# Kernel optimization log

Hardware: AMD Instinct MI355X
Metric: run time of the kernel (lower is better)

## Reference

```python
import jax, jax.numpy as jnp
import numpy as np

N = 50000
NEG_SLOPE = 0.2  # PyG GATConv default negative_slope


def _gat_layer(x, src, dst, edge_attr, W, We, a_src, a_dst, a_edge, bias):
    """Single-head PyG GATConv (heads=1, concat=True, add_self_loops=True,
    fill_value='mean' for self-loop edge_attr, dropout inactive / eval mode)."""
    n = x.shape[0]
    # add self loops; self-loop edge_attr = per-feature mean of edge_attr
    loop = jnp.arange(n)
    src2 = jnp.concatenate([src, loop])
    dst2 = jnp.concatenate([dst, loop])
    ea_loop = jnp.broadcast_to(edge_attr.mean(axis=0, keepdims=True), (n, edge_attr.shape[1]))
    ea = jnp.concatenate([edge_attr, ea_loop], axis=0)          # [E', edge_dim]

    h = x @ W                                                    # [N, C_out]
    a_s = h @ a_src                                              # [N]
    a_d = h @ a_dst                                              # [N]
    a_e = (ea @ We) @ a_edge                                     # [E']

    alpha = jax.nn.leaky_relu(a_s[src2] + a_d[dst2] + a_e, NEG_SLOPE)  # [E']
    # segment softmax over incoming edges of each dst node
    amax = jax.ops.segment_max(alpha, dst2, num_segments=n)     # [N]
    ex = jnp.exp(alpha - amax[dst2])                             # [E']
    denom = jax.ops.segment_sum(ex, dst2, num_segments=n)       # [N]
    w = ex / denom[dst2]                                         # [E']

    msg = h[src2] * w[:, None]                                   # [E', C_out]
    out = jax.ops.segment_sum(msg, dst2, num_segments=n) + bias  # [N, C_out]
    return out


def setup_inputs() -> dict:
    key = jax.random.key(0)
    ks = jax.random.split(key, 16)
    E, C_in, C_h, C_out, Ed = 800000, 128, 256, 128, 8
    s = 0.05
    inp = {
        "x": jax.random.normal(ks[0], (N, C_in), dtype=jnp.float32),
        "edge_index": jax.random.randint(ks[1], (2, E), 0, N, dtype=jnp.int32),
        "edge_attr": jax.random.normal(ks[2], (E, Ed), dtype=jnp.float32),
        # layer 1 params
        "W1": jax.random.normal(ks[3], (C_in, C_h), dtype=jnp.float32) * s,
        "We1": jax.random.normal(ks[4], (Ed, C_h), dtype=jnp.float32) * s,
        "as1": jax.random.normal(ks[5], (C_h,), dtype=jnp.float32) * s,
        "ad1": jax.random.normal(ks[6], (C_h,), dtype=jnp.float32) * s,
        "ae1": jax.random.normal(ks[7], (C_h,), dtype=jnp.float32) * s,
        "b1": jnp.zeros((C_h,), dtype=jnp.float32),
        # layer 2 params
        "W2": jax.random.normal(ks[8], (C_h, C_out), dtype=jnp.float32) * s,
        "We2": jax.random.normal(ks[9], (Ed, C_out), dtype=jnp.float32) * s,
        "as2": jax.random.normal(ks[10], (C_out,), dtype=jnp.float32) * s,
        "ad2": jax.random.normal(ks[11], (C_out,), dtype=jnp.float32) * s,
        "ae2": jax.random.normal(ks[12], (C_out,), dtype=jnp.float32) * s,
        "b2": jnp.zeros((C_out,), dtype=jnp.float32),
    }
    return inp


def reference(x, edge_index, edge_attr, W1, We1, as1, ad1, ae1, b1,
              W2, We2, as2, ad2, ae2, b2):
    src, dst = edge_index[0], edge_index[1]
    h = _gat_layer(x, src, dst, edge_attr, W1, We1, as1, ad1, ae1, b1)
    h = jax.nn.relu(h)  # relu between layers, not after last
    out = _gat_layer(h, src, dst, edge_attr, W2, We2, as2, ad2, ae2, b2)
    return out
```

## Files before the change

kernel.cpp:

```cpp
#include <hip/hip_runtime.h>
#include <hip/hip_bf16.h>


#define NEG_SLOPE 0.2f

typedef unsigned short u16;
typedef short short8 __attribute__((ext_vector_type(8)));
typedef float v4f __attribute__((ext_vector_type(4)));
typedef u16 u16x4 __attribute__((ext_vector_type(4)));
typedef u16 u16x8 __attribute__((ext_vector_type(8)));

__device__ __forceinline__ u16 f2bf(float f) {
    unsigned u = __float_as_uint(f);
    return (u16)((u + 0x7fffu + ((u >> 16) & 1u)) >> 16);
}
__device__ __forceinline__ float bf2f(u16 h) {
    return __uint_as_float(((unsigned)h) << 16);
}
__device__ __forceinline__ float bf_lo(int v) { return __uint_as_float(((unsigned)v) << 16); }
__device__ __forceinline__ float bf_hi(int v) { return __uint_as_float(((unsigned)v) & 0xffff0000u); }
__device__ __forceinline__ float lrelu(float x) {
    return x >= 0.f ? x : NEG_SLOPE * x;
}
__device__ __forceinline__ int ld_acq(int* p) {
    return __hip_atomic_load(p, __ATOMIC_ACQUIRE, __HIP_MEMORY_SCOPE_AGENT);
}
__device__ __forceinline__ void st_rel(int* p, int v) {
    __hip_atomic_store(p, v, __ATOMIC_RELEASE, __HIP_MEMORY_SCOPE_AGENT);
}

__global__ __launch_bounds__(256) void prep_kernel(
        const float* __restrict__ W1, u16* __restrict__ w1thi, u16* __restrict__ w1tlo,
        const float* __restrict__ W2, u16* __restrict__ w2thi, u16* __restrict__ w2tlo,
        const float* __restrict__ We1, const float* __restrict__ ae1v,
        const float* __restrict__ We2, const float* __restrict__ ae2v,
        float* __restrict__ we_vec1g, float* __restrict__ we_vec2g) {
    int tid = threadIdx.x;
    if (blockIdx.x < 256) {
        int t = blockIdx.x * 256 + tid;
        if (t < 128 * 256) {
            int k = t >> 8, m = t & 255;
            float v = W1[t];
            u16 h = f2bf(v);
            w1thi[(size_t)m * 128 + k] = h;
            w1tlo[(size_t)m * 128 + k] = f2bf(v - bf2f(h));
        } else {
            t -= 128 * 256;
            int k = t >> 7, m = t & 127;
            float v = W2[t];
            u16 h = f2bf(v);
            w2thi[(size_t)m * 256 + k] = h;
            w2tlo[(size_t)m * 256 + k] = f2bf(v - bf2f(h));
        }
        return;
    }
    __shared__ float wv[16];
    if (tid < 16) wv[tid] = 0.f;
    __syncthreads();
    {
        float a1 = ae1v[tid];
        int lane = tid & 63;
#pragma unroll
        for (int j = 0; j < 8; ++j) {
            float v = We1[j * 256 + tid] * a1;
#pragma unroll
            for (int o = 32; o; o >>= 1) v += __shfl_down(v, o);
            if (lane == 0) atomicAdd(&wv[j], v);
        }
        if (tid < 128) {
            float a2 = ae2v[tid];
#pragma unroll
            for (int j = 0; j < 8; ++j) {
                float v = We2[j * 128 + tid] * a2;
#pragma unroll
                for (int o = 32; o; o >>= 1) v += __shfl_down(v, o);
                if (lane == 0) atomicAdd(&wv[8 + j], v);
            }
        }
    }
    __syncthreads();
    if (tid < 8)  we_vec1g[tid] = wv[tid];
    else if (tid < 16) we_vec2g[tid - 8] = wv[tid];
}

#define BK 32
#define LDA 40
__global__ __launch_bounds__(256) void fat1_kernel(
        const float* __restrict__ ea, const int* __restrict__ dst,
        float* __restrict__ mean_acc, int* __restrict__ deg,
        int* __restrict__ rank, float2* __restrict__ aEe, int E,
        const float* __restrict__ we_vec1g, const float* __restrict__ we_vec2g,
        int Fb,
        const float* __restrict__ A32,
        const u16* __restrict__ Bh_g, const u16* __restrict__ Bl_g,
        u16* __restrict__ Cb, int Nrows, int K, int M,
        const float* __restrict__ av, const float* __restrict__ bv,
        float* __restrict__ as_out, float* __restrict__ ad_out, int gx) {
    __shared__ u16 Ah[64 * LDA], Bh[64 * LDA], Bl[64 * LDA];
    int tid = threadIdx.x;
    if ((int)blockIdx.x < Fb) {
        __shared__ float red[8];
        __shared__ float wv[16];
        if (tid < 16) { wv[tid] = (tid < 8) ? we_vec1g[tid] : we_vec2g[tid - 8];
                        if (tid < 8) red[tid] = 0.f; }
        __syncthreads();
        int e = (int)blockIdx.x * 256 + tid;
        float s[8] = {0.f};
        if (e < E) {
            const float4 v0 = *(const float4*)&ea[(size_t)e * 8];
            const float4 v1 = *(const float4*)&ea[(size_t)e * 8 + 4];
            int d = dst[e];
            s[0] = v0.x; s[1] = v0.y; s[2] = v0.z; s[3] = v0.w;
            s[4] = v1.x; s[5] = v1.y; s[6] = v1.z; s[7] = v1.w;
            float s1 = v0.x * wv[0] + v0.y * wv[1] + v0.z * wv[2] + v0.w * wv[3]
                     + v1.x * wv[4] + v1.y * wv[5] + v1.z * wv[6] + v1.w * wv[7];
            float s2 = v0.x * wv[8] + v0.y * wv[9] + v0.z * wv[10] + v0.w * wv[11]
                     + v1.x * wv[12] + v1.y * wv[13] + v1.z * wv[14] + v1.w * wv[15];
            aEe[e] = make_float2(s1, s2);
            rank[e] = atomicAdd(&deg[d << 4], 1);
        }
        int lane = tid & 63;
#pragma unroll
        for (int j = 0; j < 8; ++j) {
#pragma unroll
            for (int o = 32; o; o >>= 1) s[j] += __shfl_down(s[j], o);
            if (lane == 0) atomicAdd(&red[j], s[j]);
        }
        __syncthreads();
        if (tid < 8) atomicAdd(&mean_acc[tid], red[tid]);
        return;
    }
    int gb = (int)blockIdx.x - Fb;
    int lane = tid & 63;
    int wvx = tid >> 6;
    int l15 = lane & 15, quad = lane >> 4;
    int rb = (gb / gx) * 64;
    int cb = (gb % gx) * 64;

    v4f acc[4];
#pragma unroll
    for (int ni = 0; ni < 4; ++ni) acc[ni] = (v4f){0.f, 0.f, 0.f, 0.f};

    int sr = tid >> 2;
    int sc = (tid & 3) * 8;

    for (int kc = 0; kc < K; kc += BK) {
        int gr = rb + sr;
        u16x8 a0 = {0,0,0,0,0,0,0,0};
        if (gr < Nrows) {
            const float* pa = A32 + (size_t)gr * K + kc + sc;
            float4 f0 = *(const float4*)pa;
            float4 f1 = *(const float4*)(pa + 4);
            a0 = (u16x8){f2bf(f0.x), f2bf(f0.y), f2bf(f0.z), f2bf(f0.w),
                         f2bf(f1.x), f2bf(f1.y), f2bf(f1.z), f2bf(f1.w)};
        }
        size_t bb = (size_t)(cb + sr) * K + kc + sc;
        u16x8 b0 = *(const u16x8*)(Bh_g + bb);
        u16x8 b1 = *(const u16x8*)(Bl_g + bb);
        *(u16x8*)&Ah[sr * LDA + sc] = a0;
        *(u16x8*)&Bh[sr * LDA + sc] = b0;
        *(u16x8*)&Bl[sr * LDA + sc] = b1;
        __syncthreads();
        short8 ah = *(const short8*)&Ah[(wvx * 16 + l15) * LDA + quad * 8];
        short8 bh[4], bl[4];
#pragma unroll
        for (int ni = 0; ni < 4; ++ni) {
            int r = (ni * 16 + l15) * LDA + quad * 8;
            bh[ni] = *(const short8*)&Bh[r];
            bl[ni] = *(const short8*)&Bl[r];
        }
#pragma unroll
        for (int ni = 0; ni < 4; ++ni) {
            acc[ni] = __builtin_amdgcn_mfma_f32_16x16x32_bf16(ah, bh[ni], acc[ni], 0, 0, 0);
            acc[ni] = __builtin_amdgcn_mfma_f32_16x16x32_bf16(ah, bl[ni], acc[ni], 0, 0, 0);
        }
        __syncthreads();
    }
#pragma unroll
    for (int ni = 0; ni < 4; ++ni)
#pragma unroll
        for (int reg = 0; reg < 4; ++reg) {
            int row = rb + wvx * 16 + quad * 4 + reg;
            if (row < Nrows)
                Cb[(size_t)row * M + cb + ni * 16 + l15] = f2bf(acc[ni][reg]);
        }
    float sd[4] = {}, dd[4] = {};
#pragma unroll
    for (int ni = 0; ni < 4; ++ni) {
        int col = cb + ni * 16 + l15;
        float a = av[col], b = bv[col];
#pragma unroll
        for (int reg = 0; reg < 4; ++reg) {
            sd[reg] += acc[ni][reg] * a;
            dd[reg] += acc[ni][reg] * b;
        }
    }
#pragma unroll
    for (int off = 1; off < 16; off <<= 1)
#pragma unroll
        for (int reg = 0; reg < 4; ++reg) {
            sd[reg] += __shfl_xor(sd[reg], off);
            dd[reg] += __shfl_xor(dd[reg], off);
        }
    if (l15 == 0) {
        int row0 = rb + wvx * 16 + quad * 4;
#pragma unroll
        for (int reg = 0; reg < 4; ++reg)
            if (row0 + reg < Nrows) {
                atomicAdd(as_out + row0 + reg, sd[reg]);
                atomicAdd(ad_out + row0 + reg, dd[reg]);
            }
    }
}

__global__ __launch_bounds__(256) void scan_fused_kernel(
        const int* __restrict__ deg, int* __restrict__ row_start,
        int* __restrict__ partials, int* __restrict__ pprefix,
        int* __restrict__ gcount, int* __restrict__ gflag, int N, int n,
        const float* __restrict__ mean_acc, float Einv,
        const float* __restrict__ we_vec1, const float* __restrict__ we_vec2,
        float* __restrict__ ae_loop) {
    __shared__ int s[256];
    __shared__ int amLast, bprefix;
    int t = threadIdx.x, bid = blockIdx.x;
    int i = bid * 256 + t;
    int v = (i < N) ? deg[i << 4] : 0;
    s[t] = v; __syncthreads();
    for (int off = 1; off < 256; off <<= 1) {
        int u = (t >= off) ? s[t - off] : 0;
        __syncthreads();
        s[t] += u;
        __syncthreads();
    }
    int incl = s[t];
    int total = s[255];
    if (t == 0) {
        partials[bid] = total;
        __threadfence();
        int c = __hip_atomic_fetch_add(gcount, 1, __ATOMIC_ACQ_REL, __HIP_MEMORY_SCOPE_AGENT);
        amLast = (c == (int)gridDim.x - 1);
    }
    __syncthreads();
    if (amLast) {
        int G = gridDim.x;
        int pv = (t < G) ? ld_acq(&partials[t]) : 0;
        __syncthreads();
        s[t] = pv; __syncthreads();
        for (int off = 1; off < 256; off <<= 1) {
            int u = (t >= off) ? s[t - off] : 0;
            __syncthreads();
            s[t] += u;
            __syncthreads();
        }
        if (t < G) pprefix[t] = s[t] - pv;
        if (t == 0) {
            float s1 = 0.f, s2 = 0.f;
#pragma unroll
            for (int j = 0; j < 8; ++j) {
                float m = mean_acc[j] * Einv;
                s1 += m * we_vec1[j];
                s2 += m * we_vec2[j];
            }
            ae_loop[0] = s1; ae_loop[1] = s2;
        }
        __threadfence();
        __syncthreads();
        if (t == 0) st_rel(gflag, 1);
    }
    if (t == 0) {
        while (ld_acq(gflag) == 0) __builtin_amdgcn_s_sleep(2);
        bprefix = ld_acq(&pprefix[bid]);
    }
    __syncthreads();
    int ex = bprefix + incl - v;
    if (i < n) row_start[i] = ex;
}

__global__ __launch_bounds__(256) void fill_kernel(
        const int* __restrict__ src, const int* __restrict__ dst,
        const float2* __restrict__ aEe, const int* __restrict__ row_start,
        const int* __restrict__ rank,
        float4* __restrict__ epack, int E) {
    int e = blockIdx.x * 256 + threadIdx.x;
    if (e >= E) return;
    int d = dst[e];
    int idx = row_start[d] + rank[e];
    float2 a = aEe[e];
    epack[idx] = make_float4(__int_as_float(src[e]), a.x, a.y, 0.f);
}

#define LDA2 40
__global__ __launch_bounds__(256) void gemm_mfma_kernel(
        const u16* __restrict__ A_g,
        const u16* __restrict__ Bh_g, const u16* __restrict__ Bl_g,
        u16* __restrict__ Cb, int Nrows, int K, int M,
        const float* __restrict__ av, const float* __restrict__ bv,
        float* __restrict__ as_out, float* __restrict__ ad_out) {
    __shared__ u16 Ah[128 * LDA2], Bh[128 * LDA2], Bl[128 * LDA2];
    int tid = threadIdx.x;
    int lane = tid & 63;
    int wv = tid >> 6;
    int wm = wv >> 1, wn = wv & 1;
    int l15 = lane & 15, quad = lane >> 4;
    int rb = blockIdx.y * 128;
    int cb = blockIdx.x * 128;

    v4f acc[4][4];
#pragma unroll
    for (int mi = 0; mi < 4; ++mi)
#pragma unroll
        for (int ni = 0; ni < 4; ++ni) acc[mi][ni] = (v4f){0.f, 0.f, 0.f, 0.f};

    int sr = tid >> 1;
    int sc = (tid & 1) * 16;

    for (int kc = 0; kc < K; kc += BK) {
        int gr = rb + sr;
        u16x8 a0 = {0,0,0,0,0,0,0,0}, a1 = {0,0,0,0,0,0,0,0};
        if (gr < Nrows) {
            size_t ba = (size_t)gr * K + kc + sc;
            a0 = *(const u16x8*)(A_g + ba);
            a1 = *(const u16x8*)(A_g + ba + 8);
        }
        size_t bb = (size_t)(cb + sr) * K + kc + sc;
        u16x8 b0 = *(const u16x8*)(Bh_g + bb);
        u16x8 b1 = *(const u16x8*)(Bh_g + bb + 8);
        u16x8 b2 = *(const u16x8*)(Bl_g + bb);
        u16x8 b3 = *(const u16x8*)(Bl_g + bb + 8);
        *(u16x8*)&Ah[sr * LDA2 + sc] = a0;
        *(u16x8*)&Ah[sr * LDA2 + sc + 8] = a1;
        *(u16x8*)&Bh[sr * LDA2 + sc] = b0;
        *(u16x8*)&Bh[sr * LDA2 + sc + 8] = b1;
        *(u16x8*)&Bl[sr * LDA2 + sc] = b2;
        *(u16x8*)&Bl[sr * LDA2 + sc + 8] = b3;
        __syncthreads();
        short8 ah[4], bh[4], bl[4];
#pragma unroll
        for (int mi = 0; mi < 4; ++mi)
            ah[mi] = *(const short8*)&Ah[(wm * 64 + mi * 16 + l15) * LDA2 + quad * 8];
#pragma unroll
        for (int ni = 0; ni < 4; ++ni) {
            int r = (wn * 64 + ni * 16 + l15) * LDA2 + quad * 8;
            bh[ni] = *(const short8*)&Bh[r];
            bl[ni] = *(const short8*)&Bl[r];
        }
#pragma unroll
        for (int mi = 0; mi < 4; ++mi)
#pragma unroll
            for (int ni = 0; ni < 4; ++ni) {
                acc[mi][ni] = __builtin_amdgcn_mfma_f32_16x16x32_bf16(ah[mi], bh[ni], acc[mi][ni], 0, 0, 0);
                acc[mi][ni] = __builtin_amdgcn_mfma_f32_16x16x32_bf16(ah[mi], bl[ni], acc[mi][ni], 0, 0, 0);
            }
        __syncthreads();
    }
#pragma unroll
    for (int mi = 0; mi < 4; ++mi)
#pragma unroll
        for (int ni = 0; ni < 4; ++ni)
#pragma unroll
            for (int reg = 0; reg < 4; ++reg) {
                int row = rb + wm * 64 + mi * 16 + quad * 4 + reg;
                if (row < Nrows)
                    Cb[(size_t)row * M + cb + wn * 64 + ni * 16 + l15] = f2bf(acc[mi][ni][reg]);
            }
    float sd[4][4] = {}, dd[4][4] = {};
#pragma unroll
    for (int ni = 0; ni < 4; ++ni) {
        int col = cb + wn * 64 + ni * 16 + l15;
        float a = av[col], b = bv[col];
#pragma unroll
        for (int mi = 0; mi < 4; ++mi)
#pragma unroll
            for (int reg = 0; reg < 4; ++reg) {
                sd[mi][reg] += acc[mi][ni][reg] * a;
                dd[mi][reg] += acc[mi][ni][reg] * b;
            }
    }
#pragma unroll
    for (int off = 1; off < 16; off <<= 1)
#pragma unroll
        for (int mi = 0; mi < 4; ++mi)
#pragma unroll
            for (int reg = 0; reg < 4; ++reg) {
                sd[mi][reg] += __shfl_xor(sd[mi][reg], off);
                dd[mi][reg] += __shfl_xor(dd[mi][reg], off);
            }
    if (l15 == 0)
#pragma unroll
        for (int mi = 0; mi < 4; ++mi) {
            int row0 = rb + wm * 64 + mi * 16 + quad * 4;
#pragma unroll
            for (int reg = 0; reg < 4; ++reg)
                if (row0 + reg < Nrows) {
                    atomicAdd(as_out + row0 + reg, sd[mi][reg]);
                    atomicAdd(ad_out + row0 + reg, dd[mi][reg]);
                }
        }
}

__global__ __launch_bounds__(256) void agg1_kernel(const int* __restrict__ row_start,
                                                   const float4* __restrict__ epack,
                                                   const float* __restrict__ asv,
                                                   const float* __restrict__ adv,
                                                   const float* __restrict__ ae_loop,
                                                   const u16* __restrict__ Hb,
                                                   u16* __restrict__ ohi,
                                                   const float* __restrict__ bias, int N) {
    __shared__ float2 xch[4][64];
    int lane = threadIdx.x & 63;
    int wvi = threadIdx.x >> 6;
    int node = blockIdx.x * 4 + wvi;
    if (node >= N) return;
    int st = row_start[node], en = row_start[node + 1];
    float ad = adv[node];
    float aloop = lrelu(asv[node] + ad + ae_loop[0]);
    float m = aloop, sum = 1.f;
    float acc0, acc1, acc2, acc3;
    {
        int2 hv = *(const int2*)(Hb + (size_t)node * 256 + lane * 4);
        acc0 = bf_lo(hv.x); acc1 = bf_hi(hv.x);
        acc2 = bf_lo(hv.y); acc3 = bf_hi(hv.y);
    }
    for (int base = st; base < en; base += 64) {
        int i = base + lane;
        float al = -3.0e38f; int sreg = 0;
        if (i < en) {
            float4 ep = epack[i];
            sreg = __float_as_int(ep.x);
            al = lrelu(asv[sreg] + ad + ep.y);
        }
        float cm = al;
#pragma unroll
        for (int o = 1; o < 64; o <<= 1) cm = fmaxf(cm, __shfl_xor(cm, o));
        if (cm > m) {
            float sc = __expf(m - cm);
            acc0 *= sc; acc1 *= sc; acc2 *= sc; acc3 *= sc;
            sum *= sc; m = cm;
        }
        float w = (i < en) ? __expf(al - m) : 0.f;
        float wsum = w;
#pragma unroll
        for (int o = 1; o < 64; o <<= 1) wsum += __shfl_xor(wsum, o);
        sum += wsum;
        xch[wvi][lane] = make_float2(w, __int_as_float(sreg));
        int cnt = min(64, en - base);
        int j = 0;
        for (; j + 8 <= cnt; j += 8) {
            float2 e[8]; int2 h[8];
#pragma unroll
            for (int q = 0; q < 8; ++q) e[q] = xch[wvi][j + q];
#pragma unroll
            for (int q = 0; q < 8; ++q)
                h[q] = *(const int2*)(Hb + (size_t)__float_as_int(e[q].y) * 256 + lane * 4);
#pragma unroll
            for (int q = 0; q < 8; ++q) {
                acc0 += e[q].x * bf_lo(h[q].x); acc1 += e[q].x * bf_hi(h[q].x);
                acc2 += e[q].x * bf_lo(h[q].y); acc3 += e[q].x * bf_hi(h[q].y);
            }
        }
        for (; j + 4 <= cnt; j += 4) {
            float2 e0 = xch[wvi][j], e1 = xch[wvi][j + 1];
            float2 e2 = xch[wvi][j + 2], e3 = xch[wvi][j + 3];
            int2 h0 = *(const int2*)(Hb + (size_t)__float_as_int(e0.y) * 256 + lane * 4);
            int2 h1 = *(const int2*)(Hb + (size_t)__float_as_int(e1.y) * 256 + lane * 4);
            int2 h2 = *(const int2*)(Hb + (size_t)__float_as_int(e2.y) * 256 + lane * 4);
            int2 h3 = *(const int2*)(Hb + (size_t)__float_as_int(e3.y) * 256 + lane * 4);
            acc0 += e0.x * bf_lo(h0.x) + e1.x * bf_lo(h1.x) + e2.x * bf_lo(h2.x) + e3.x * bf_lo(h3.x);
            acc1 += e0.x * bf_hi(h0.x) + e1.x * bf_hi(h1.x) + e2.x * bf_hi(h2.x) + e3.x * bf_hi(h3.x);
            acc2 += e0.x * bf_lo(h0.y) + e1.x * bf_lo(h1.y) + e2.x * bf_lo(h2.y) + e3.x * bf_lo(h3.y);
            acc3 += e0.x * bf_hi(h0.y) + e1.x * bf_hi(h1.y) + e2.x * bf_hi(h2.y) + e3.x * bf_hi(h3.y);
        }
        for (; j < cnt; ++j) {
            float2 e0 = xch[wvi][j];
            int2 h0 = *(const int2*)(Hb + (size_t)__float_as_int(e0.y) * 256 + lane * 4);
            acc0 += e0.x * bf_lo(h0.x); acc1 += e0.x * bf_hi(h0.x);
            acc2 += e0.x * bf_lo(h0.y); acc3 += e0.x * bf_hi(h0.y);
        }
    }
    float inv = 1.f / sum;
    const float4 bvv = *(const float4*)(bias + lane * 4);
    float t0 = acc0 * inv + bvv.x, t1 = acc1 * inv + bvv.y;
    float t2 = acc2 * inv + bvv.z, t3 = acc3 * inv + bvv.w;
    t0 = t0 > 0.f ? t0 : 0.f; t1 = t1 > 0.f ? t1 : 0.f;
    t2 = t2 > 0.f ? t2 : 0.f; t3 = t3 > 0.f ? t3 : 0.f;
    u16x4 h;
    h.x = f2bf(t0); h.y = f2bf(t1); h.z = f2bf(t2); h.w = f2bf(t3);
    *(u16x4*)(ohi + (size_t)node * 256 + lane * 4) = h;
}

__global__ __launch_bounds__(256) void agg2_kernel(const int* __restrict__ row_start,
                                                   const float4* __restrict__ epack,
                                                   const float* __restrict__ asv,
                                                   const float* __restrict__ adv,
                                                   const float* __restrict__ ae_loop,
                                                   const u16* __restrict__ Hb,
                                                   float* __restrict__ out,
                                                   const float* __restrict__ bias, int N) {
    __shared__ float2 xch[4][64];
    int lane = threadIdx.x & 63;
    int wvi = threadIdx.x >> 6;
    int node = blockIdx.x * 4 + wvi;
    if (node >= N) return;
    int st = row_start[node], en = row_start[node + 1];
    float ad = adv[node];
    float aloop = lrelu(asv[node] + ad + ae_loop[1]);
    float m = aloop, sum = 1.f;
    float acc0, acc1;
    {
        int hv = *(const int*)(Hb + (size_t)node * 128 + lane * 2);
        acc0 = bf_lo(hv); acc1 = bf_hi(hv);
    }
    for (int base = st; base < en; base += 64) {
        int i = base + lane;
        float al = -3.0e38f; int sreg = 0;
        if (i < en) {
            float4 ep = epack[i];
            sreg = __float_as_int(ep.x);
            al = lrelu(asv[sreg] + ad + ep.z);
        }
        float cm = al;
#pragma unroll
        for (int o = 1; o < 64; o <<= 1) cm = fmaxf(cm, __shfl_xor(cm, o));
        if (cm > m) {
            float sc = __expf(m - cm);
            acc0 *= sc; acc1 *= sc;
            sum *= sc; m = cm;
        }
        float w = (i < en) ? __expf(al - m) : 0.f;
        float wsum = w;
#pragma unroll
        for (int o = 1; o < 64; o <<= 1) wsum += __shfl_xor(wsum, o);
        sum += wsum;
        xch[wvi][lane] = make_float2(w, __int_as_float(sreg));
        int cnt = min(64, en - base);
        int j = 0;
        for (; j + 8 <= cnt; j += 8) {
            float2 e[8]; int h[8];
#pragma unroll
            for (int q = 0; q < 8; ++q) e[q] = xch[wvi][j + q];
#pragma unroll
            for (int q = 0; q < 8; ++q)
                h[q] = *(const int*)(Hb + (size_t)__float_as_int(e[q].y) * 128 + lane * 2);
#pragma unroll
            for (int q = 0; q < 8; ++q) {
                acc0 += e[q].x * bf_lo(h[q]); acc1 += e[q].x * bf_hi(h[q]);
            }
        }
        for (; j + 4 <= cnt; j += 4) {
            float2 e0 = xch[wvi][j], e1 = xch[wvi][j + 1];
            float2 e2 = xch[wvi][j + 2], e3 = xch[wvi][j + 3];
            int h0 = *(const int*)(Hb + (size_t)__float_as_int(e0.y) * 128 + lane * 2);
            int h1 = *(const int*)(Hb + (size_t)__float_as_int(e1.y) * 128 + lane * 2);
            int h2 = *(const int*)(Hb + (size_t)__float_as_int(e2.y) * 128 + lane * 2);
            int h3 = *(const int*)(Hb + (size_t)__float_as_int(e3.y) * 128 + lane * 2);
            acc0 += e0.x * bf_lo(h0) + e1.x * bf_lo(h1) + e2.x * bf_lo(h2) + e3.x * bf_lo(h3);
            acc1 += e0.x * bf_hi(h0) + e1.x * bf_hi(h1) + e2.x * bf_hi(h2) + e3.x * bf_hi(h3);
        }
        for (; j < cnt; ++j) {
            float2 e0 = xch[wvi][j];
            int h0 = *(const int*)(Hb + (size_t)__float_as_int(e0.y) * 128 + lane * 2);
            acc0 += e0.x * bf_lo(h0); acc1 += e0.x * bf_hi(h0);
        }
    }
    float inv = 1.f / sum;
    size_t o = (size_t)node * 128 + lane * 2;
    out[o]     = acc0 * inv + bias[lane * 2];
    out[o + 1] = acc1 * inv + bias[lane * 2 + 1];
}

extern "C" void kernel_launch(void* const* d_in, const int* in_sizes, int n_in,
                              void* d_out, int out_size, void* d_ws, size_t ws_size,
                              hipStream_t stream) {
    const int Cin = 128, Ch = 256, Co = 128;
    const int N = in_sizes[0] / Cin;
    const int E = in_sizes[1] / 2;

    const float* x   = (const float*)d_in[0];
    const int*   src = (const int*)d_in[1];
    const int*   dst = src + E;
    const float* ea  = (const float*)d_in[2];
    const float* W1  = (const float*)d_in[3];
    const float* We1 = (const float*)d_in[4];
    const float* as1 = (const float*)d_in[5];
    const float* ad1 = (const float*)d_in[6];
    const float* ae1 = (const float*)d_in[7];
    const float* b1  = (const float*)d_in[8];
    const float* W2  = (const float*)d_in[9];
    const float* We2 = (const float*)d_in[10];
    const float* as2 = (const float*)d_in[11];
    const float* ad2 = (const float*)d_in[12];
    const float* ae2 = (const float*)d_in[13];
    const float* b2  = (const float*)d_in[14];
    float* out = (float*)d_out;

    float* ws = (float*)d_ws;
    size_t off = 0;
    u16* h1b = (u16*)(ws + off); off += (size_t)N * Ch / 2;
    u16* g1b = (u16*)(ws + off); off += (size_t)N * Ch / 2;
    float4* epack = (float4*)(ws + off); off += (size_t)E * 4;
    float2* aEe   = (float2*)(ws + off); off += (size_t)E * 2;
    int* rank     = (int*)(ws + off); off += (size_t)E;
    int* row_start = (int*)(ws + off); off += (size_t)N + 1;
    int* partials  = (int*)(ws + off); off += 256;
    int* pprefix   = (int*)(ws + off); off += 256;
    u16* w1thi = (u16*)(ws + off); off += (size_t)Cin * Ch / 2;
    u16* w1tlo = (u16*)(ws + off); off += (size_t)Cin * Ch / 2;
    u16* w2thi = (u16*)(ws + off); off += (size_t)Ch * Co / 2;
    u16* w2tlo = (u16*)(ws + off); off += (size_t)Ch * Co / 2;
    int*   deg  = (int*)(ws + off); off += (size_t)16 * (N + 1);
    float* asv1 = ws + off; off += (size_t)N;
    float* adv1 = ws + off; off += (size_t)N;
    float* asv2 = ws + off; off += (size_t)N;
    float* adv2 = ws + off; off += (size_t)N;
    float* misc = ws + off; off += 32;
    float* mean_acc = misc;
    float* we_vec1  = misc + 8;
    float* we_vec2  = misc + 16;
    float* ae_loop  = misc + 24;
    int* gcount = (int*)(ws + off); off += 1;
    int* gflag  = (int*)(ws + off); off += 1;

    const int n1 = N + 1;
    const int nscan = (n1 + 255) / 256;

    hipMemsetAsync(deg, 0, ((size_t)20 * N + 50) * sizeof(float), stream);

    prep_kernel<<<257, 256, 0, stream>>>(
        W1, w1thi, w1tlo, W2, w2thi, w2tlo,
        We1, ae1, We2, ae2, we_vec1, we_vec2);

    {
        int Fb = (E + 255) / 256;
        int gx = Ch / 64;
        int Gg = gx * ((N + 63) / 64);
        fat1_kernel<<<Fb + Gg, 256, 0, stream>>>(
            ea, dst, mean_acc, deg, rank, aEe, E, we_vec1, we_vec2, Fb,
            x, w1thi, w1tlo, h1b, N, Cin, Ch, as1, ad1, asv1, adv1, gx);
    }

    scan_fused_kernel<<<nscan, 256, 0, stream>>>(
        deg, row_start, partials, pprefix, gcount, gflag, N, n1,
        mean_acc, 1.0f / (float)E, we_vec1, we_vec2, ae_loop);

    fill_kernel<<<(E + 255) / 256, 256, 0, stream>>>(src, dst, aEe, row_start,
                                                     rank, epack, E);

    agg1_kernel<<<(N + 3) / 4, 256, 0, stream>>>(row_start, epack, asv1, adv1, ae_loop,
                                                 h1b, g1b, b1, N);

    u16* h2b = h1b;
    {
        dim3 grid(Co / 128, (N + 127) / 128);
        gemm_mfma_kernel<<<grid, 256, 0, stream>>>(g1b, w2thi, w2tlo, h2b, N, Ch, Co,
                                                   as2, ad2, asv2, adv2);
    }
    agg2_kernel<<<(N + 3) / 4, 256, 0, stream>>>(row_start, epack, asv2, adv2, ae_loop,
                                                 h2b, out, b2, N);
}
```

Baseline: 417.4 us.

## Interleave edge and GEMM blocks, grid-stride edge pass, widen GEMM tile, unpad degrees

The fused first kernel now interleaves edge-preprocessing blocks with GEMM blocks instead of placing all edge blocks first. The edge pass uses a fixed count of 1024 blocks that walk the edges with a grid stride, which reduces block-level reductions and mean atomics. GEMM tiles are widened from 64 to 128 columns so each A tile is reused across more outputs. The degree array loses its 16-int padding, which shrinks the memset and the scan reads but lets atomics on neighbouring nodes share cache lines.

```diff
diff --git a/kernel.cpp b/kernel.cpp
--- a/kernel.cpp
+++ b/kernel.cpp
@@ -90,34 +90,46 @@
         float* __restrict__ mean_acc, int* __restrict__ deg,
         int* __restrict__ rank, float2* __restrict__ aEe, int E,
         const float* __restrict__ we_vec1g, const float* __restrict__ we_vec2g,
-        int Fb,
+        int Fb, int Gg,
         const float* __restrict__ A32,
         const u16* __restrict__ Bh_g, const u16* __restrict__ Bl_g,
         u16* __restrict__ Cb, int Nrows, int K, int M,
         const float* __restrict__ av, const float* __restrict__ bv,
         float* __restrict__ as_out, float* __restrict__ ad_out, int gx) {
-    __shared__ u16 Ah[64 * LDA], Bh[64 * LDA], Bl[64 * LDA];
+    __shared__ u16 Ah[64 * LDA];
+    __shared__ u16 Bh[128 * LDA];
+    __shared__ u16 Bl[128 * LDA];
+    __shared__ float red[8];
     int tid = threadIdx.x;
-    if ((int)blockIdx.x < Fb) {
-        __shared__ float red[8];
-        __shared__ float wv[16];
-        if (tid < 16) { wv[tid] = (tid < 8) ? we_vec1g[tid] : we_vec2g[tid - 8];
-                        if (tid < 8) red[tid] = 0.f; }
-        __syncthreads();
-        int e = (int)blockIdx.x * 256 + tid;
+    int bid = (int)blockIdx.x;
+    int mn = Fb < Gg ? Fb : Gg;
+    int hid = -1, gid = -1;
+    if (bid < 2 * mn) {
+        if ((bid & 1) == 0) hid = bid >> 1; else gid = bid >> 1;
+    } else {
+        int rem = bid - 2 * mn;
+        if (Fb > Gg) hid = mn + rem; else gid = mn + rem;
+    }
+    if (hid >= 0) {
+        float wv[16];
+#pragma unroll
+        for (int j = 0; j < 8; ++j) { wv[j] = we_vec1g[j]; wv[8 + j] = we_vec2g[j]; }
+        if (tid < 8) red[tid] = 0.f;
+        __syncthreads();
         float s[8] = {0.f};
-        if (e < E) {
+        int stride = Fb * 256;
+        for (int e = hid * 256 + tid; e < E; e += stride) {
+            int d = dst[e];
             const float4 v0 = *(const float4*)&ea[(size_t)e * 8];
             const float4 v1 = *(const float4*)&ea[(size_t)e * 8 + 4];
-            int d = dst[e];
-            s[0] = v0.x; s[1] = v0.y; s[2] = v0.z; s[3] = v0.w;
-            s[4] = v1.x; s[5] = v1.y; s[6] = v1.z; s[7] = v1.w;
+            s[0] += v0.x; s[1] += v0.y; s[2] += v0.z; s[3] += v0.w;
+            s[4] += v1.x; s[5] += v1.y; s[6] += v1.z; s[7] += v1.w;
             float s1 = v0.x * wv[0] + v0.y * wv[1] + v0.z * wv[2] + v0.w * wv[3]
                      + v1.x * wv[4] + v1.y * wv[5] + v1.z * wv[6] + v1.w * wv[7];
             float s2 = v0.x * wv[8] + v0.y * wv[9] + v0.z * wv[10] + v0.w * wv[11]
                      + v1.x * wv[12] + v1.y * wv[13] + v1.z * wv[14] + v1.w * wv[15];
             aEe[e] = make_float2(s1, s2);
-            rank[e] = atomicAdd(&deg[d << 4], 1);
+            rank[e] = atomicAdd(&deg[d], 1);
         }
         int lane = tid & 63;
 #pragma unroll
@@ -130,19 +142,20 @@
         if (tid < 8) atomicAdd(&mean_acc[tid], red[tid]);
         return;
     }
-    int gb = (int)blockIdx.x - Fb;
     int lane = tid & 63;
     int wvx = tid >> 6;
     int l15 = lane & 15, quad = lane >> 4;
-    int rb = (gb / gx) * 64;
-    int cb = (gb % gx) * 64;
-
-    v4f acc[4];
-#pragma unroll
-    for (int ni = 0; ni < 4; ++ni) acc[ni] = (v4f){0.f, 0.f, 0.f, 0.f};
-
-    int sr = tid >> 2;
-    int sc = (tid & 3) * 8;
+    int rb = (gid / gx) * 64;
+    int cb = (gid % gx) * 128;
+
+    v4f acc[8];
+#pragma unroll
+    for (int ni = 0; ni < 8; ++ni) acc[ni] = (v4f){0.f, 0.f, 0.f, 0.f};
+
+    int sr  = tid >> 2;
+    int sc  = (tid & 3) * 8;
+    int sr2 = tid >> 1;
+    int sc2 = (tid & 1) * 16;
 
     for (int kc = 0; kc < K; kc += BK) {
         int gr = rb + sr;
@@ -154,30 +167,30 @@
             a0 = (u16x8){f2bf(f0.x), f2bf(f0.y), f2bf(f0.z), f2bf(f0.w),
                          f2bf(f1.x), f2bf(f1.y), f2bf(f1.z), f2bf(f1.w)};
         }
-        size_t bb = (size_t)(cb + sr) * K + kc + sc;
+        size_t bb = (size_t)(cb + sr2) * K + kc + sc2;
         u16x8 b0 = *(const u16x8*)(Bh_g + bb);
-        u16x8 b1 = *(const u16x8*)(Bl_g + bb);
+        u16x8 b1 = *(const u16x8*)(Bh_g + bb + 8);
+        u16x8 b2 = *(const u16x8*)(Bl_g + bb);
+        u16x8 b3 = *(const u16x8*)(Bl_g + bb + 8);
         *(u16x8*)&Ah[sr * LDA + sc] = a0;
-        *(u16x8*)&Bh[sr * LDA + sc] = b0;
-        *(u16x8*)&Bl[sr * LDA + sc] = b1;
+        *(u16x8*)&Bh[sr2 * LDA + sc2] = b0;
+        *(u16x8*)&Bh[sr2 * LDA + sc2 + 8] = b1;
+        *(u16x8*)&Bl[sr2 * LDA + sc2] = b2;
+        *(u16x8*)&Bl[sr2 * LDA + sc2 + 8] = b3;
         __syncthreads();
         short8 ah = *(const short8*)&Ah[(wvx * 16 + l15) * LDA + quad * 8];
-        short8 bh[4], bl[4];
-#pragma unroll
-        for (int ni = 0; ni < 4; ++ni) {
+#pragma unroll
+        for (int ni = 0; ni < 8; ++ni) {
             int r = (ni * 16 + l15) * LDA + quad * 8;
-            bh[ni] = *(const short8*)&Bh[r];
-            bl[ni] = *(const short8*)&Bl[r];
-        }
-#pragma unroll
-        for (int ni = 0; ni < 4; ++ni) {
-            acc[ni] = __builtin_amdgcn_mfma_f32_16x16x32_bf16(ah, bh[ni], acc[ni], 0, 0, 0);
-            acc[ni] = __builtin_amdgcn_mfma_f32_16x16x32_bf16(ah, bl[ni], acc[ni], 0, 0, 0);
-        }
-        __syncthreads();
-    }
-#pragma unroll
-    for (int ni = 0; ni < 4; ++ni)
+            short8 bhf = *(const short8*)&Bh[r];
+            short8 blf = *(const short8*)&Bl[r];
+            acc[ni] = __builtin_amdgcn_mfma_f32_16x16x32_bf16(ah, bhf, acc[ni], 0, 0, 0);
+            acc[ni] = __builtin_amdgcn_mfma_f32_16x16x32_bf16(ah, blf, acc[ni], 0, 0, 0);
+        }
+        __syncthreads();
+    }
+#pragma unroll
+    for (int ni = 0; ni < 8; ++ni)
 #pragma unroll
         for (int reg = 0; reg < 4; ++reg) {
             int row = rb + wvx * 16 + quad * 4 + reg;
@@ -186,7 +199,7 @@
         }
     float sd[4] = {}, dd[4] = {};
 #pragma unroll
-    for (int ni = 0; ni < 4; ++ni) {
+    for (int ni = 0; ni < 8; ++ni) {
         int col = cb + ni * 16 + l15;
         float a = av[col], b = bv[col];
 #pragma unroll
@@ -224,7 +237,7 @@
     __shared__ int amLast, bprefix;
     int t = threadIdx.x, bid = blockIdx.x;
     int i = bid * 256 + t;
-    int v = (i < N) ? deg[i << 4] : 0;
+    int v = (i < N) ? deg[i] : 0;
     s[t] = v; __syncthreads();
     for (int off = 1; off < 256; off <<= 1) {
         int u = (t >= off) ? s[t - off] : 0;
@@ -607,7 +620,7 @@
     u16* w1tlo = (u16*)(ws + off); off += (size_t)Cin * Ch / 2;
     u16* w2thi = (u16*)(ws + off); off += (size_t)Ch * Co / 2;
     u16* w2tlo = (u16*)(ws + off); off += (size_t)Ch * Co / 2;
-    int*   deg  = (int*)(ws + off); off += (size_t)16 * (N + 1);
+    int*   deg  = (int*)(ws + off); off += (size_t)N + 1;
     float* asv1 = ws + off; off += (size_t)N;
     float* adv1 = ws + off; off += (size_t)N;
     float* asv2 = ws + off; off += (size_t)N;
@@ -623,18 +636,18 @@
     const int n1 = N + 1;
     const int nscan = (n1 + 255) / 256;
 
-    hipMemsetAsync(deg, 0, ((size_t)20 * N + 50) * sizeof(float), stream);
+    hipMemsetAsync(deg, 0, ((size_t)5 * N + 35) * sizeof(float), stream);
 
     prep_kernel<<<257, 256, 0, stream>>>(
         W1, w1thi, w1tlo, W2, w2thi, w2tlo,
         We1, ae1, We2, ae2, we_vec1, we_vec2);
 
     {
-        int Fb = (E + 255) / 256;
-        int gx = Ch / 64;
+        int Fb = 1024;
+        int gx = Ch / 128;
         int Gg = gx * ((N + 63) / 64);
         fat1_kernel<<<Fb + Gg, 256, 0, stream>>>(
-            ea, dst, mean_acc, deg, rank, aEe, E, we_vec1, we_vec2, Fb,
+            ea, dst, mean_acc, deg, rank, aEe, E, we_vec1, we_vec2, Fb, Gg,
             x, w1thi, w1tlo, h1b, N, Cin, Ch, as1, ad1, asv1, adv1, gx);
     }
 
```

Result: faster. 349.8 us (-16.2%).
